# Optimization experiments

Hardware: AMD Instinct MI355X
Metric: run time of the kernel (lower is better)

## Reference

```python
import jax, jax.numpy as jnp
import numpy as np

BS, N, DX, DE, DY, NH = 4, 256, 256, 64, 64, 8
DF = DX // NH


def setup_inputs() -> dict:
    key = jax.random.key(0)
    ks = jax.random.split(key, 24)

    def w(k, i, o):
        return jax.random.normal(k, (i, o), jnp.float32) / jnp.sqrt(jnp.float32(i))

    d = {}
    d["x"] = jax.random.normal(ks[0], (BS, N, DX), jnp.float32)
    d["e"] = jax.random.normal(ks[1], (BS, N, N, DE), jnp.float32)
    d["y"] = jax.random.normal(ks[2], (BS, DY), jnp.float32)
    d["node_mask"] = jnp.ones((BS, N), jnp.float32)
    # projections (use_bias=False in the module)
    d["Wq"] = w(ks[3], DX, DX)
    d["Wk"] = w(ks[4], DX, DX)
    d["Wv"] = w(ks[5], DX, DX)
    d["We_mul"] = w(ks[6], DE, DX)
    d["We_add"] = w(ks[7], DE, DX)
    d["Wye_add"] = w(ks[8], DY, DX)
    d["Wye_mul"] = w(ks[9], DY, DX)
    d["Wyx_add"] = w(ks[10], DY, DX)
    d["Wyx_mul"] = w(ks[11], DY, DX)
    d["Wyy"] = w(ks[12], DY, DY)
    # pooled-feature -> y maps (Xtoy / Etoy use 4*d features: mean,min,max,std)
    d["Wxy"] = w(ks[13], 4 * DX, DY)
    d["bxy"] = jnp.zeros((DY,), jnp.float32)
    d["Wey"] = w(ks[14], 4 * DE, DY)
    d["bey"] = jnp.zeros((DY,), jnp.float32)
    # output heads (bias=True, flax Dense default)
    d["We_out"] = w(ks[15], DX, DE)
    d["be_out"] = jnp.zeros((DE,), jnp.float32)
    d["Wx_out"] = w(ks[16], DX, DX)
    d["bx_out"] = jnp.zeros((DX,), jnp.float32)
    d["Wy_out"] = w(ks[17], DY, DY)
    d["by_out"] = jnp.zeros((DY,), jnp.float32)
    return d


def reference(x, e, y, node_mask, Wq, Wk, Wv, We_mul, We_add, Wye_add, Wye_mul,
              Wyx_add, Wyx_mul, Wyy, Wxy, bxy, Wey, bey, We_out, be_out,
              Wx_out, bx_out, Wy_out, by_out):
    bs, n, dx = x.shape
    nh, df = NH, DF
    x_mask = node_mask[..., None]                       # (bs,n,1)
    e_mask1 = x_mask[:, :, None, :]                     # (bs,n,1,1)
    e_mask2 = x_mask[:, None, :, :]                     # (bs,1,n,1)
    em = e_mask1 * e_mask2                              # (bs,n,n,1)

    q = (x @ Wq) * x_mask
    k = (x @ Wk) * x_mask
    Q = q.reshape(bs, n, 1, nh, df)                     # (bs,n,1,h,df)
    K = k.reshape(bs, 1, n, nh, df)                     # (bs,1,n,h,df)
    Y = Q * K / jnp.sqrt(jnp.float32(df))               # (bs,n,n,h,df) per-channel scores

    e1 = ((e @ We_mul) * em).reshape(bs, n, n, nh, df)
    e2 = ((e @ We_add) * em).reshape(bs, n, n, nh, df)
    Y = Y * (e1 + 1.0) + e2                             # FiLM by edges

    newE = Y.reshape(bs, n, n, dx)
    ye1 = (y @ Wye_add)[:, None, None, :]
    ye2 = (y @ Wye_mul)[:, None, None, :]
    newE = ye1 + (ye2 + 1.0) * newE                     # FiLM by global y
    newE = (newE @ We_out + be_out) * em                # (bs,n,n,de)

    # masked softmax over key axis (axis=2); mask broadcasts over df
    mask5 = e_mask2[..., None] > 0                      # (bs,1,n,1,1)
    attn = jax.nn.softmax(jnp.where(mask5, Y, -1e9), axis=2)

    v = ((x @ Wv) * x_mask).reshape(bs, 1, n, nh, df)
    weighted = (attn * v).sum(axis=2).reshape(bs, n, dx)

    yx1 = (y @ Wyx_add)[:, None, :]
    yx2 = (y @ Wyx_mul)[:, None, :]
    newX = yx1 + (yx2 + 1.0) * weighted
    newX = (newX @ Wx_out + bx_out) * x_mask            # (bs,n,dx)

    def pool(t, axes):
        return jnp.concatenate([t.mean(axis=axes), t.min(axis=axes),
                                t.max(axis=axes), t.std(axis=axes, ddof=1)], axis=-1)

    x_y = pool(x, (1,)) @ Wxy + bxy                     # (bs,dy)
    e_y = pool(e, (1, 2)) @ Wey + bey                   # (bs,dy)
    y_y = y @ Wyy
    newY = (y_y + e_y + x_y) @ Wy_out + by_out          # (bs,dy)
    return newX, newE, newY
```

## Files before the change

kernel.cpp:

```cpp
#include <hip/hip_runtime.h>
#include <hip/hip_bf16.h>

#define BSZ 4
#define NN  256
#define DXX 256
#define DEE 64
#define DYY 64

#define OFF_Q     0
#define OFF_K     262144
#define OFF_V     524288
#define OFF_XW    786432
#define OFF_YE1   1048576
#define OFF_YE2   1049600
#define OFF_YX1   1050624
#define OFF_YX2   1051648
#define OFF_PX    1052672
#define OFF_EPART 1057792

typedef __attribute__((ext_vector_type(8))) short bf16x8;
typedef __attribute__((ext_vector_type(4))) float f32x4;

__device__ __forceinline__ short f2bf(float f) {
    unsigned u = __float_as_uint(f);
    unsigned r = u + 0x7fffu + ((u >> 16) & 1u);
    return (short)(r >> 16);
}

__device__ __forceinline__ unsigned cvt_pk_bf16(float lo, float hi) {
    unsigned r;
    asm("v_cvt_pk_bf16_f32 %0, %1, %2" : "=v"(r) : "v"(lo), "v"(hi));
    return r;
}

__device__ __forceinline__ void pack8_store(const float4& A, const float4& B, short* dst) {
    uint4 v;
    v.x = cvt_pk_bf16(A.x, A.y);
    v.y = cvt_pk_bf16(A.z, A.w);
    v.z = cvt_pk_bf16(B.x, B.y);
    v.w = cvt_pk_bf16(B.z, B.w);
    *(uint4*)dst = v;
}

__global__ __launch_bounds__(256) void prep_kernel(
    const float* __restrict__ x, const float* __restrict__ e, const float* __restrict__ y,
    const float* __restrict__ nm,
    const float* __restrict__ Wq, const float* __restrict__ Wk, const float* __restrict__ Wv,
    const float* __restrict__ Wye_add, const float* __restrict__ Wye_mul,
    const float* __restrict__ Wyx_add, const float* __restrict__ Wyx_mul,
    float* __restrict__ ws) {

    __shared__ float smem[16 * 256];
    const int blk = blockIdx.x;
    const int t = threadIdx.x;

    if (blk < 384) {
        const int which = blk >> 7;
        const int m0 = (blk & 127) * 8;
        const float* W = which == 0 ? Wq : (which == 1 ? Wk : Wv);
        float* out = ws + (size_t)which * 262144;
        float (*xl)[256] = (float(*)[256])smem;
        for (int r = 0; r < 8; ++r) xl[r][t] = x[(m0 + r) * 256 + t];
        __syncthreads();
        float acc[8];
#pragma unroll
        for (int r = 0; r < 8; ++r) acc[r] = 0.f;
        for (int d = 0; d < 256; d += 4) {
            float w0 = W[(d + 0) * 256 + t];
            float w1 = W[(d + 1) * 256 + t];
            float w2 = W[(d + 2) * 256 + t];
            float w3 = W[(d + 3) * 256 + t];
#pragma unroll
            for (int r = 0; r < 8; ++r) {
                float4 ev = *(const float4*)&xl[r][d];
                acc[r] = fmaf(ev.x, w0, fmaf(ev.y, w1, fmaf(ev.z, w2, fmaf(ev.w, w3, acc[r]))));
            }
        }
        if (which == 0) {
#pragma unroll
            for (int r = 0; r < 8; ++r) {
                int m = m0 + r;
                out[m * 256 + t] = acc[r] * nm[m];
            }
        } else {
            const int bb2  = m0 >> 8;
            const int jloc = m0 & 255;
            float tv[8];
#pragma unroll
            for (int r = 0; r < 8; ++r) tv[r] = acc[r] * nm[m0 + r];
            float* outb = out + (size_t)bb2 * 65536 + t * 256 + jloc;
            *(float4*)&outb[0] = make_float4(tv[0], tv[1], tv[2], tv[3]);
            *(float4*)&outb[4] = make_float4(tv[4], tv[5], tv[6], tv[7]);
        }
    } else if (blk < 388) {
        const int b = blk - 384;
        float a1 = 0.f, a2 = 0.f, a3 = 0.f, a4 = 0.f;
        for (int k = 0; k < DYY; ++k) {
            float yv = y[b * DYY + k];
            a1 = fmaf(yv, Wye_add[k * 256 + t], a1);
            a2 = fmaf(yv, Wye_mul[k * 256 + t], a2);
            a3 = fmaf(yv, Wyx_add[k * 256 + t], a3);
            a4 = fmaf(yv, Wyx_mul[k * 256 + t], a4);
        }
        ws[OFF_YE1 + b * 256 + t] = a1;
        ws[OFF_YE2 + b * 256 + t] = a2;
        ws[OFF_YX1 + b * 256 + t] = a3;
        ws[OFF_YX2 + b * 256 + t] = a4;
    } else if (blk < 644) {
        const int idx = blk - 388;
        const int s = idx & 63, bb = idx >> 6;
        const int dq = (t & 15) * 4, g = t >> 4;
        const float* base = e + ((size_t)bb * 65536 + s * 1024) * 64;
        float s0 = 0.f, s1 = 0.f, s2 = 0.f, s3 = 0.f;
        float q0 = 0.f, q1 = 0.f, q2 = 0.f, q3 = 0.f;
        float mn0 = 1e30f, mn1 = 1e30f, mn2 = 1e30f, mn3 = 1e30f;
        float mx0 = -1e30f, mx1 = -1e30f, mx2 = -1e30f, mx3 = -1e30f;
#pragma unroll 4
        for (int rr = 0; rr < 64; ++rr) {
            const int row = g * 64 + rr;
            float4 v = *(const float4*)&base[row * 64 + dq];
            s0 += v.x; s1 += v.y; s2 += v.z; s3 += v.w;
            q0 = fmaf(v.x, v.x, q0); q1 = fmaf(v.y, v.y, q1);
            q2 = fmaf(v.z, v.z, q2); q3 = fmaf(v.w, v.w, q3);
            mn0 = fminf(mn0, v.x); mn1 = fminf(mn1, v.y);
            mn2 = fminf(mn2, v.z); mn3 = fminf(mn3, v.w);
            mx0 = fmaxf(mx0, v.x); mx1 = fmaxf(mx1, v.y);
            mx2 = fmaxf(mx2, v.z); mx3 = fmaxf(mx3, v.w);
        }
        float (*red)[16][64] = (float(*)[16][64])smem;
        red[0][g][dq + 0] = s0;  red[0][g][dq + 1] = s1;  red[0][g][dq + 2] = s2;  red[0][g][dq + 3] = s3;
        red[1][g][dq + 0] = q0;  red[1][g][dq + 1] = q1;  red[1][g][dq + 2] = q2;  red[1][g][dq + 3] = q3;
        red[2][g][dq + 0] = mn0; red[2][g][dq + 1] = mn1; red[2][g][dq + 2] = mn2; red[2][g][dq + 3] = mn3;
        red[3][g][dq + 0] = mx0; red[3][g][dq + 1] = mx1; red[3][g][dq + 2] = mx2; red[3][g][dq + 3] = mx3;
        __syncthreads();
        const int stat = t >> 6, d = t & 63;
        float a;
        if (stat < 2) {
            a = 0.f;
            for (int gg = 0; gg < 16; ++gg) a += red[stat][gg][d];
        } else if (stat == 2) {
            a = 1e30f;
            for (int gg = 0; gg < 16; ++gg) a = fminf(a, red[2][gg][d]);
        } else {
            a = -1e30f;
            for (int gg = 0; gg < 16; ++gg) a = fmaxf(a, red[3][gg][d]);
        }
        ws[OFF_EPART + (size_t)((bb * 64 + s) * 64 + d) * 4 + stat] = a;
    } else {
        const int b = blk - 644;
        float s = 0.f, q = 0.f, mn = 1e30f, mx = -1e30f;
        for (int i = 0; i < 256; ++i) {
            float v = x[(b * 256 + i) * 256 + t];
            s += v; q = fmaf(v, v, q);
            mn = fminf(mn, v); mx = fmaxf(mx, v);
        }
        float mean = s * (1.f / 256.f);
        float var  = (q - s * s * (1.f / 256.f)) * (1.f / 255.f);
        var = fmaxf(var, 0.f);
        ws[OFF_PX + b * 1024 + t]       = mean;
        ws[OFF_PX + b * 1024 + 256 + t] = mn;
        ws[OFF_PX + b * 1024 + 512 + t] = mx;
        ws[OFF_PX + b * 1024 + 768 + t] = sqrtf(var);
    }
}

#define EBP  72
#define YPLP 264

__global__ __launch_bounds__(256, 2) void fusedmfma_kernel(
    const float* __restrict__ e, const float* __restrict__ nmask,
    const float* __restrict__ Wm, const float* __restrict__ Wa,
    const float* __restrict__ We_out, const float* __restrict__ be_out,
    const float* __restrict__ ws, float* __restrict__ outE, float* __restrict__ xw) {

    const int i = blockIdx.x, b = blockIdx.y;
    const int tid  = threadIdx.x;
    const int w    = tid >> 6;
    const int lane = tid & 63;
    const int quad = lane >> 4, l16 = lane & 15;

    __shared__ __align__(16) short ebuf[2][32 * EBP];
    __shared__ __align__(16) short ypl[2][32 * YPLP];
    __shared__ float nml[256];

    nml[tid] = nmask[b * 256 + tid];

    bf16x8 bm[4][2], ba[4][2], bw[8];
    const int cw = w * 64;
#pragma unroll
    for (int ct = 0; ct < 4; ++ct) {
        const int c = cw + ct * 16 + l16;
#pragma unroll
        for (int s = 0; s < 2; ++s) {
            bf16x8 t1, t2;
#pragma unroll
            for (int jj = 0; jj < 8; ++jj) {
                const int d = s * 32 + quad * 8 + jj;
                t1[jj] = f2bf(Wm[d * 256 + c]);
                t2[jj] = f2bf(Wa[d * 256 + c]);
            }
            bm[ct][s] = t1; ba[ct][s] = t2;
        }
    }
    const int cp = w * 16 + l16;
    {
#pragma unroll
        for (int s = 0; s < 8; ++s) {
            bf16x8 t;
#pragma unroll
            for (int jj = 0; jj < 8; ++jj) {
                const int cch = s * 32 + quad * 8 + jj;
                t[jj] = f2bf(We_out[cch * 64 + cp]);
            }
            bw[s] = t;
        }
    }
    const float bo = be_out[cp];

    const float rs = 0.17677669529663687f;
    float qc[4], ye1c[4], ye2c[4];
#pragma unroll
    for (int ct = 0; ct < 4; ++ct) {
        const int c = cw + ct * 16 + l16;
        qc[ct]   = ws[OFF_Q + (size_t)(b * 256 + i) * 256 + c] * rs;
        ye1c[ct] = ws[OFF_YE1 + b * 256 + c];
        ye2c[ct] = ws[OFF_YE2 + b * 256 + c] + 1.f;
    }
    const float* kTb = ws + OFF_K + (size_t)b * 65536;
    const float* vTb = ws + OFF_V + (size_t)b * 65536;

    const float* eb = e + ((size_t)(b * 256 + i)) * 256 * 64;
    const int jr = tid >> 3, c0 = (tid & 7) * 8;
    {
        float4 A = *(const float4*)(eb + jr * 64 + c0);
        float4 B = *(const float4*)(eb + jr * 64 + c0 + 4);
        pack8_store(A, B, &ebuf[0][jr * EBP + c0]);
    }
    __syncthreads();
    const float mi = nml[i];
    const size_t outbase = (size_t)(b * 256 + i) * 256;

    float msm[4], lsm[4], wsm[4];
#pragma unroll
    for (int ct = 0; ct < 4; ++ct) { msm[ct] = -1e30f; lsm[ct] = 0.f; wsm[ct] = 0.f; }

    for (int chunk = 0; chunk < 8; ++chunk) {
        const int cur = chunk & 1, j0 = chunk * 32;

        float4 pfA, pfB;
        if (chunk < 7) {
            const float* nb = eb + (size_t)(j0 + 32 + jr) * 64 + c0;
            pfA = *(const float4*)(nb);
            pfB = *(const float4*)(nb + 4);
        }

        bf16x8 ae[2][2];
#pragma unroll
        for (int jt = 0; jt < 2; ++jt)
#pragma unroll
            for (int s = 0; s < 2; ++s)
                ae[jt][s] = *(const bf16x8*)&ebuf[cur][(jt * 16 + l16) * EBP + s * 32 + quad * 8];

        float emv[8];
#pragma unroll
        for (int jt = 0; jt < 2; ++jt)
#pragma unroll
            for (int r = 0; r < 4; ++r)
                emv[jt * 4 + r] = mi * nml[j0 + jt * 16 + quad * 4 + r];

#pragma unroll
        for (int ct = 0; ct < 4; ++ct) {
            const int c = cw + ct * 16 + l16;

            const float4 K0 = *(const float4*)&kTb[c * 256 + j0 + quad * 4];
            const float4 K1 = *(const float4*)&kTb[c * 256 + j0 + 16 + quad * 4];
            const float4 V0 = *(const float4*)&vTb[c * 256 + j0 + quad * 4];
            const float4 V1 = *(const float4*)&vTb[c * 256 + j0 + 16 + quad * 4];
            const float Ks[8] = {K0.x, K0.y, K0.z, K0.w, K1.x, K1.y, K1.z, K1.w};
            const float Vs[8] = {V0.x, V0.y, V0.z, V0.w, V1.x, V1.y, V1.z, V1.w};

            f32x4 a1_0 = {0.f, 0.f, 0.f, 0.f}, a1_1 = {0.f, 0.f, 0.f, 0.f};
            f32x4 a2_0 = {0.f, 0.f, 0.f, 0.f}, a2_1 = {0.f, 0.f, 0.f, 0.f};
#pragma unroll
            for (int s = 0; s < 2; ++s) {
                a1_0 = __builtin_amdgcn_mfma_f32_16x16x32_bf16(ae[0][s], bm[ct][s], a1_0, 0, 0, 0);
                a1_1 = __builtin_amdgcn_mfma_f32_16x16x32_bf16(ae[1][s], bm[ct][s], a1_1, 0, 0, 0);
                a2_0 = __builtin_amdgcn_mfma_f32_16x16x32_bf16(ae[0][s], ba[ct][s], a2_0, 0, 0, 0);
                a2_1 = __builtin_amdgcn_mfma_f32_16x16x32_bf16(ae[1][s], ba[ct][s], a2_1, 0, 0, 0);
            }

            float Ys[8];
#pragma unroll
            for (int jt = 0; jt < 2; ++jt) {
                float yv[4];
#pragma unroll
                for (int r = 0; r < 4; ++r) {
                    const int u  = jt * 4 + r;
                    const float e1v = (jt == 0) ? a1_0[r] : a1_1[r];
                    const float e2v = (jt == 0) ? a2_0[r] : a2_1[r];
                    const float em = emv[u];
                    const float Yv = fmaf(qc[ct] * Ks[u], fmaf(e1v, em, 1.f), e2v * em);
                    yv[r] = fmaf(ye2c[ct], Yv, ye1c[ct]);
                    Ys[u] = (em > 0.f) ? Yv : -1e9f;
                }
                const int jl0 = jt * 16 + quad * 4;
                unsigned short* yb = (unsigned short*)&ypl[cur][jl0 * YPLP + c];
                const unsigned p01 = cvt_pk_bf16(yv[0], yv[1]);
                const unsigned p23 = cvt_pk_bf16(yv[2], yv[3]);
                yb[0]        = (unsigned short)p01;
                yb[YPLP]     = (unsigned short)(p01 >> 16);
                yb[2 * YPLP] = (unsigned short)p23;
                yb[3 * YPLP] = (unsigned short)(p23 >> 16);
            }
            float cm = Ys[0];
#pragma unroll
            for (int u = 1; u < 8; ++u) cm = fmaxf(cm, Ys[u]);
            const float mnew = fmaxf(msm[ct], cm);
            const float al = __expf(msm[ct] - mnew);
            float sum = 0.f, wsum = 0.f;
#pragma unroll
            for (int u = 0; u < 8; ++u) {
                const float p = __expf(Ys[u] - mnew);
                sum += p; wsum = fmaf(p, Vs[u], wsum);
            }
            lsm[ct] = fmaf(lsm[ct], al, sum);
            wsm[ct] = fmaf(wsm[ct], al, wsum);
            msm[ct] = mnew;
        }

        if (chunk < 7) pack8_store(pfA, pfB, &ebuf[cur ^ 1][jr * EBP + c0]);
        __syncthreads();

        f32x4 acc0 = {0.f, 0.f, 0.f, 0.f}, acc1 = {0.f, 0.f, 0.f, 0.f};
#pragma unroll
        for (int s = 0; s < 8; ++s) {
            bf16x8 a0 = *(const bf16x8*)&ypl[cur][(l16) * YPLP + s * 32 + quad * 8];
            bf16x8 a1 = *(const bf16x8*)&ypl[cur][(16 + l16) * YPLP + s * 32 + quad * 8];
            acc0 = __builtin_amdgcn_mfma_f32_16x16x32_bf16(a0, bw[s], acc0, 0, 0, 0);
            acc1 = __builtin_amdgcn_mfma_f32_16x16x32_bf16(a1, bw[s], acc1, 0, 0, 0);
        }
#pragma unroll
        for (int jt = 0; jt < 2; ++jt)
#pragma unroll
            for (int r = 0; r < 4; ++r) {
                const int jl = jt * 16 + quad * 4 + r;
                const int jg = j0 + jl;
                const float em2 = mi * nml[jg];
                const float av = (jt == 0) ? acc0[r] : acc1[r];
                outE[(outbase + jg) * 64 + cp] = (av + bo) * em2;
            }
    }

#pragma unroll
    for (int ct = 0; ct < 4; ++ct) {
        float m = msm[ct], l = lsm[ct], wv = wsm[ct];
#pragma unroll
        for (int off = 16; off < 64; off <<= 1) {
            const float m2 = __shfl_xor(m, off, 64);
            const float l2 = __shfl_xor(l, off, 64);
            const float w2 = __shfl_xor(wv, off, 64);
            const float mn = fmaxf(m, m2);
            const float s1 = __expf(m - mn), s2 = __expf(m2 - mn);
            l = l * s1 + l2 * s2;
            wv = wv * s1 + w2 * s2;
            m = mn;
        }
        if (quad == 0) {
            const int c = cw + ct * 16 + l16;
            const float weighted = wv / l;
            const float yx1 = ws[OFF_YX1 + b * 256 + c];
            const float yx2 = ws[OFF_YX2 + b * 256 + c] + 1.f;
            xw[(size_t)(b * 256 + i) * 256 + c] = fmaf(yx2, weighted, yx1);
        }
    }
}

__global__ __launch_bounds__(256) void post_kernel(
    const float* __restrict__ xwin, const float* __restrict__ Wx_out,
    const float* __restrict__ bx_out, const float* __restrict__ nm,
    const float* __restrict__ y,
    const float* __restrict__ Wyy, const float* __restrict__ Wxy,
    const float* __restrict__ bxy, const float* __restrict__ Wey,
    const float* __restrict__ bey, const float* __restrict__ Wy_out,
    const float* __restrict__ by_out,
    const float* __restrict__ ws, float* __restrict__ outX, float* __restrict__ outY) {

    __shared__ float smem[16 * 256];
    const int blk = blockIdx.x;
    const int t = threadIdx.x;

    if (blk < 128) {
        const int m0 = blk * 8;
        float (*xl)[256] = (float(*)[256])smem;
        for (int r = 0; r < 8; ++r) xl[r][t] = xwin[(m0 + r) * 256 + t];
        __syncthreads();
        float acc[8];
#pragma unroll
        for (int r = 0; r < 8; ++r) acc[r] = 0.f;
        for (int d = 0; d < 256; d += 4) {
            float w0 = Wx_out[(d + 0) * 256 + t];
            float w1 = Wx_out[(d + 1) * 256 + t];
            float w2 = Wx_out[(d + 2) * 256 + t];
            float w3 = Wx_out[(d + 3) * 256 + t];
#pragma unroll
            for (int r = 0; r < 8; ++r) {
                float4 ev = *(const float4*)&xl[r][d];
                acc[r] = fmaf(ev.x, w0, fmaf(ev.y, w1, fmaf(ev.z, w2, fmaf(ev.w, w3, acc[r]))));
            }
        }
        const float bv = bx_out[t];
#pragma unroll
        for (int r = 0; r < 8; ++r) {
            int m = m0 + r;
            outX[m * 256 + t] = (acc[r] + bv) * nm[m];
        }
    } else {
        const int b = blk - 128;
        const int d = t & 63, g = t >> 6;
        {
            float S = 0.f, Q = 0.f, Mn = 1e30f, Mx = -1e30f;
            for (int ss = g * 16; ss < g * 16 + 16; ++ss) {
                const float* ep = ws + OFF_EPART + ((b * 64 + ss) * 64 + d) * 4;
                float4 p = *(const float4*)ep;
                S += p.x; Q += p.y; Mn = fminf(Mn, p.z); Mx = fmaxf(Mx, p.w);
            }
            float (*red)[4][64] = (float(*)[4][64])smem;
            red[0][g][d] = S; red[1][g][d] = Q; red[2][g][d] = Mn; red[3][g][d] = Mx;
        }
        __syncthreads();
        float* pe = smem + 1024;
        if (g == 0) {
            float (*red)[4][64] = (float(*)[4][64])smem;
            float S = 0.f, Q = 0.f, Mn = 1e30f, Mx = -1e30f;
#pragma unroll
            for (int gg = 0; gg < 4; ++gg) {
                S += red[0][gg][d]; Q += red[1][gg][d];
                Mn = fminf(Mn, red[2][gg][d]); Mx = fmaxf(Mx, red[3][gg][d]);
            }
            const float n = 65536.f;
            float meane = S / n;
            float vare  = (Q - S * S / n) / (n - 1.f);
            vare = fmaxf(vare, 0.f);
            pe[d]       = meane;
            pe[64 + d]  = Mn;
            pe[128 + d] = Mx;
            pe[192 + d] = sqrtf(vare);
        }
        __syncthreads();
        const int o = t & 63, ks = t >> 6;
        float a = 0.f;
        if (ks == 0) {
            a = bxy[o] + bey[o];
            for (int k = 0; k < 64; ++k) a = fmaf(y[b * 64 + k], Wyy[k * 64 + o], a);
        }
        for (int k = ks * 64; k < ks * 64 + 64; ++k) a = fmaf(pe[k], Wey[k * 64 + o], a);
        const float* px = ws + OFF_PX + b * 1024;
        for (int k = ks * 256; k < ks * 256 + 256; ++k) a = fmaf(px[k], Wxy[k * 64 + o], a);
        float* redB = smem + 1280;
        redB[ks * 64 + o] = a;
        __syncthreads();
        float* sy = smem + 1536;
        if (ks == 0) sy[o] = redB[o] + redB[64 + o] + redB[128 + o] + redB[192 + o];
        __syncthreads();
        if (t < 64) {
            float r = by_out[t];
            for (int k = 0; k < 64; ++k) r = fmaf(sy[k], Wy_out[k * 64 + t], r);
            outY[b * 64 + t] = r;
        }
    }
}

extern "C" void kernel_launch(void* const* d_in, const int* in_sizes, int n_in,
                              void* d_out, int out_size, void* d_ws, size_t ws_size,
                              hipStream_t stream) {
    const float* x        = (const float*)d_in[0];
    const float* e        = (const float*)d_in[1];
    const float* y        = (const float*)d_in[2];
    const float* nm       = (const float*)d_in[3];
    const float* Wq       = (const float*)d_in[4];
    const float* Wk       = (const float*)d_in[5];
    const float* Wv       = (const float*)d_in[6];
    const float* We_mul   = (const float*)d_in[7];
    const float* We_add   = (const float*)d_in[8];
    const float* Wye_add  = (const float*)d_in[9];
    const float* Wye_mul  = (const float*)d_in[10];
    const float* Wyx_add  = (const float*)d_in[11];
    const float* Wyx_mul  = (const float*)d_in[12];
    const float* Wyy      = (const float*)d_in[13];
    const float* Wxy      = (const float*)d_in[14];
    const float* bxy      = (const float*)d_in[15];
    const float* Wey      = (const float*)d_in[16];
    const float* bey      = (const float*)d_in[17];
    const float* We_out   = (const float*)d_in[18];
    const float* be_out   = (const float*)d_in[19];
    const float* Wx_out   = (const float*)d_in[20];
    const float* bx_out   = (const float*)d_in[21];
    const float* Wy_out   = (const float*)d_in[22];
    const float* by_out   = (const float*)d_in[23];

    float* ws   = (float*)d_ws;
    float* outX = (float*)d_out;
    float* outE = (float*)d_out + 262144;
    float* outY = (float*)d_out + 262144 + 16777216;

    prep_kernel<<<648, 256, 0, stream>>>(x, e, y, nm, Wq, Wk, Wv,
                                         Wye_add, Wye_mul, Wyx_add, Wyx_mul, ws);
    fusedmfma_kernel<<<dim3(256, 4), 256, 0, stream>>>(e, nm, We_mul, We_add, We_out, be_out,
                                                       ws, outE, ws + OFF_XW);
    post_kernel<<<132, 256, 0, stream>>>(ws + OFF_XW, Wx_out, bx_out, nm, y,
                                         Wyy, Wxy, bxy, Wey, bey, Wy_out, by_out,
                                         ws, outX, outY);
}
```

Measured before the change: 268.2 us.

## Fuse edge pooling statistics into the main MFMA kernel with atomic reduction

Removes the separate pass over the 64MB edge tensor in the prep kernel that computed sum, sum of squares, min and max. These statistics are now accumulated from the e tiles the fused kernel already loads, reduced per block in shared memory, and merged globally with float atomicAdd and order-preserving unsigned atomicMin/Max. The second full read of e goes away. In exchange the fused kernel needs extra registers, which may hurt occupancy, and the atomic float sums make the result order-dependent.

After: 361.8 us. 34.9% more time.

```diff
diff --git a/kernel.cpp b/kernel.cpp
--- a/kernel.cpp
+++ b/kernel.cpp
@@ -42,6 +42,14 @@
     *(uint4*)dst = v;
 }
 
+__device__ __forceinline__ unsigned encf(float f) {
+    unsigned u = __float_as_uint(f);
+    return (u >> 31) ? ~u : (u | 0x80000000u);
+}
+__device__ __forceinline__ float decf(unsigned u) {
+    return __uint_as_float((u >> 31) ? (u & 0x7fffffffu) : ~u);
+}
+
 __global__ __launch_bounds__(256) void prep_kernel(
     const float* __restrict__ x, const float* __restrict__ e, const float* __restrict__ y,
     const float* __restrict__ nm,
@@ -106,48 +114,8 @@
         ws[OFF_YE2 + b * 256 + t] = a2;
         ws[OFF_YX1 + b * 256 + t] = a3;
         ws[OFF_YX2 + b * 256 + t] = a4;
-    } else if (blk < 644) {
-        const int idx = blk - 388;
-        const int s = idx & 63, bb = idx >> 6;
-        const int dq = (t & 15) * 4, g = t >> 4;
-        const float* base = e + ((size_t)bb * 65536 + s * 1024) * 64;
-        float s0 = 0.f, s1 = 0.f, s2 = 0.f, s3 = 0.f;
-        float q0 = 0.f, q1 = 0.f, q2 = 0.f, q3 = 0.f;
-        float mn0 = 1e30f, mn1 = 1e30f, mn2 = 1e30f, mn3 = 1e30f;
-        float mx0 = -1e30f, mx1 = -1e30f, mx2 = -1e30f, mx3 = -1e30f;
-#pragma unroll 4
-        for (int rr = 0; rr < 64; ++rr) {
-            const int row = g * 64 + rr;
-            float4 v = *(const float4*)&base[row * 64 + dq];
-            s0 += v.x; s1 += v.y; s2 += v.z; s3 += v.w;
-            q0 = fmaf(v.x, v.x, q0); q1 = fmaf(v.y, v.y, q1);
-            q2 = fmaf(v.z, v.z, q2); q3 = fmaf(v.w, v.w, q3);
-            mn0 = fminf(mn0, v.x); mn1 = fminf(mn1, v.y);
-            mn2 = fminf(mn2, v.z); mn3 = fminf(mn3, v.w);
-            mx0 = fmaxf(mx0, v.x); mx1 = fmaxf(mx1, v.y);
-            mx2 = fmaxf(mx2, v.z); mx3 = fmaxf(mx3, v.w);
-        }
-        float (*red)[16][64] = (float(*)[16][64])smem;
-        red[0][g][dq + 0] = s0;  red[0][g][dq + 1] = s1;  red[0][g][dq + 2] = s2;  red[0][g][dq + 3] = s3;
-        red[1][g][dq + 0] = q0;  red[1][g][dq + 1] = q1;  red[1][g][dq + 2] = q2;  red[1][g][dq + 3] = q3;
-        red[2][g][dq + 0] = mn0; red[2][g][dq + 1] = mn1; red[2][g][dq + 2] = mn2; red[2][g][dq + 3] = mn3;
-        red[3][g][dq + 0] = mx0; red[3][g][dq + 1] = mx1; red[3][g][dq + 2] = mx2; red[3][g][dq + 3] = mx3;
-        __syncthreads();
-        const int stat = t >> 6, d = t & 63;
-        float a;
-        if (stat < 2) {
-            a = 0.f;
-            for (int gg = 0; gg < 16; ++gg) a += red[stat][gg][d];
-        } else if (stat == 2) {
-            a = 1e30f;
-            for (int gg = 0; gg < 16; ++gg) a = fminf(a, red[2][gg][d]);
-        } else {
-            a = -1e30f;
-            for (int gg = 0; gg < 16; ++gg) a = fmaxf(a, red[3][gg][d]);
-        }
-        ws[OFF_EPART + (size_t)((bb * 64 + s) * 64 + d) * 4 + stat] = a;
-    } else {
-        const int b = blk - 644;
+    } else if (blk < 392) {
+        const int b = blk - 388;
         float s = 0.f, q = 0.f, mn = 1e30f, mx = -1e30f;
         for (int i = 0; i < 256; ++i) {
             float v = x[(b * 256 + i) * 256 + t];
@@ -161,17 +129,29 @@
         ws[OFF_PX + b * 1024 + 256 + t] = mn;
         ws[OFF_PX + b * 1024 + 512 + t] = mx;
         ws[OFF_PX + b * 1024 + 768 + t] = sqrtf(var);
+    } else {
+        float* ep = ws + OFF_EPART;
+        ep[t]       = 0.f;
+        ep[256 + t] = 0.f;
+        ((unsigned*)ep)[512 + t] = 0u;
+        ((unsigned*)ep)[768 + t] = 0xFFFFFFFFu;
     }
 }
 
 #define EBP  72
 #define YPLP 264
+
+#define ESTAT(k, v) { es[k] += (v); eq[k] = fmaf((v), (v), eq[k]); \
+                      emn[k] = fminf(emn[k], (v)); emx[k] = fmaxf(emx[k], (v)); }
+#define ESTAT8(A, B) { ESTAT(0, A.x) ESTAT(1, A.y) ESTAT(2, A.z) ESTAT(3, A.w) \
+                       ESTAT(4, B.x) ESTAT(5, B.y) ESTAT(6, B.z) ESTAT(7, B.w) }
 
 __global__ __launch_bounds__(256, 2) void fusedmfma_kernel(
     const float* __restrict__ e, const float* __restrict__ nmask,
     const float* __restrict__ Wm, const float* __restrict__ Wa,
     const float* __restrict__ We_out, const float* __restrict__ be_out,
-    const float* __restrict__ ws, float* __restrict__ outE, float* __restrict__ xw) {
+    const float* __restrict__ ws, float* __restrict__ outE, float* __restrict__ xw,
+    float* __restrict__ epart) {
 
     const int i = blockIdx.x, b = blockIdx.y;
     const int tid  = threadIdx.x;
@@ -229,11 +209,16 @@
     const float* kTb = ws + OFF_K + (size_t)b * 65536;
     const float* vTb = ws + OFF_V + (size_t)b * 65536;
 
+    float es[8], eq[8], emn[8], emx[8];
+#pragma unroll
+    for (int k = 0; k < 8; ++k) { es[k] = 0.f; eq[k] = 0.f; emn[k] = 1e30f; emx[k] = -1e30f; }
+
     const float* eb = e + ((size_t)(b * 256 + i)) * 256 * 64;
     const int jr = tid >> 3, c0 = (tid & 7) * 8;
     {
         float4 A = *(const float4*)(eb + jr * 64 + c0);
         float4 B = *(const float4*)(eb + jr * 64 + c0 + 4);
+        ESTAT8(A, B)
         pack8_store(A, B, &ebuf[0][jr * EBP + c0]);
     }
     __syncthreads();
@@ -328,7 +313,10 @@
             msm[ct] = mnew;
         }
 
-        if (chunk < 7) pack8_store(pfA, pfB, &ebuf[cur ^ 1][jr * EBP + c0]);
+        if (chunk < 7) {
+            ESTAT8(pfA, pfB)
+            pack8_store(pfA, pfB, &ebuf[cur ^ 1][jr * EBP + c0]);
+        }
         __syncthreads();
 
         f32x4 acc0 = {0.f, 0.f, 0.f, 0.f}, acc1 = {0.f, 0.f, 0.f, 0.f};
@@ -349,6 +337,30 @@
                 const float av = (jt == 0) ? acc0[r] : acc1[r];
                 outE[(outbase + jg) * 64 + cp] = (av + bo) * em2;
             }
+    }
+
+    __syncthreads();
+    {
+        float* sred = (float*)ypl;
+        const int cg = tid & 7;
+        const int jr2 = tid >> 3;
+#pragma unroll
+        for (int k = 0; k < 8; ++k)
+            *(float4*)&sred[jr2 * 260 + (cg * 8 + k) * 4] =
+                make_float4(es[k], eq[k], emn[k], emx[k]);
+        __syncthreads();
+        if (tid < 64) {
+            float4 a = make_float4(0.f, 0.f, 1e30f, -1e30f);
+            for (int j = 0; j < 32; ++j) {
+                float4 v = *(const float4*)&sred[j * 260 + tid * 4];
+                a.x += v.x; a.y += v.y;
+                a.z = fminf(a.z, v.z); a.w = fmaxf(a.w, v.w);
+            }
+            atomicAdd(&epart[b * 64 + tid], a.x);
+            atomicAdd(&epart[256 + b * 64 + tid], a.y);
+            atomicMax((unsigned*)epart + 512 + b * 64 + tid, encf(a.w));
+            atomicMin((unsigned*)epart + 768 + b * 64 + tid, encf(a.z));
+        }
     }
 
 #pragma unroll
@@ -416,35 +428,20 @@
         }
     } else {
         const int b = blk - 128;
-        const int d = t & 63, g = t >> 6;
-        {
-            float S = 0.f, Q = 0.f, Mn = 1e30f, Mx = -1e30f;
-            for (int ss = g * 16; ss < g * 16 + 16; ++ss) {
-                const float* ep = ws + OFF_EPART + ((b * 64 + ss) * 64 + d) * 4;
-                float4 p = *(const float4*)ep;
-                S += p.x; Q += p.y; Mn = fminf(Mn, p.z); Mx = fmaxf(Mx, p.w);
-            }
-            float (*red)[4][64] = (float(*)[4][64])smem;
-            red[0][g][d] = S; red[1][g][d] = Q; red[2][g][d] = Mn; red[3][g][d] = Mx;
-        }
-        __syncthreads();
-        float* pe = smem + 1024;
-        if (g == 0) {
-            float (*red)[4][64] = (float(*)[4][64])smem;
-            float S = 0.f, Q = 0.f, Mn = 1e30f, Mx = -1e30f;
-#pragma unroll
-            for (int gg = 0; gg < 4; ++gg) {
-                S += red[0][gg][d]; Q += red[1][gg][d];
-                Mn = fminf(Mn, red[2][gg][d]); Mx = fmaxf(Mx, red[3][gg][d]);
-            }
+        float* pe = smem;
+        if (t < 64) {
+            const float* ep = ws + OFF_EPART;
+            const float S = ep[b * 64 + t];
+            const float Q = ep[256 + b * 64 + t];
+            const unsigned mxe = ((const unsigned*)ep)[512 + b * 64 + t];
+            const unsigned mne = ((const unsigned*)ep)[768 + b * 64 + t];
             const float n = 65536.f;
             float meane = S / n;
-            float vare  = (Q - S * S / n) / (n - 1.f);
-            vare = fmaxf(vare, 0.f);
-            pe[d]       = meane;
-            pe[64 + d]  = Mn;
-            pe[128 + d] = Mx;
-            pe[192 + d] = sqrtf(vare);
+            float vare  = fmaxf((Q - S * S / n) / (n - 1.f), 0.f);
+            pe[t]       = meane;
+            pe[64 + t]  = decf(mne);
+            pe[128 + t] = decf(mxe);
+            pe[192 + t] = sqrtf(vare);
         }
         __syncthreads();
         const int o = t & 63, ks = t >> 6;
@@ -456,10 +453,10 @@
         for (int k = ks * 64; k < ks * 64 + 64; ++k) a = fmaf(pe[k], Wey[k * 64 + o], a);
         const float* px = ws + OFF_PX + b * 1024;
         for (int k = ks * 256; k < ks * 256 + 256; ++k) a = fmaf(px[k], Wxy[k * 64 + o], a);
-        float* redB = smem + 1280;
+        float* redB = smem + 256;
         redB[ks * 64 + o] = a;
         __syncthreads();
-        float* sy = smem + 1536;
+        float* sy = smem + 512;
         if (ks == 0) sy[o] = redB[o] + redB[64 + o] + redB[128 + o] + redB[192 + o];
         __syncthreads();
         if (t < 64) {
@@ -503,10 +500,11 @@
     float* outE = (float*)d_out + 262144;
     float* outY = (float*)d_out + 262144 + 16777216;
 
-    prep_kernel<<<648, 256, 0, stream>>>(x, e, y, nm, Wq, Wk, Wv,
+    prep_kernel<<<393, 256, 0, stream>>>(x, e, y, nm, Wq, Wk, Wv,
                                          Wye_add, Wye_mul, Wyx_add, Wyx_mul, ws);
     fusedmfma_kernel<<<dim3(256, 4), 256, 0, stream>>>(e, nm, We_mul, We_add, We_out, be_out,
-                                                       ws, outE, ws + OFF_XW);
+                                                       ws, outE, ws + OFF_XW,
+                                                       ws + OFF_EPART);
     post_kernel<<<132, 256, 0, stream>>>(ws + OFF_XW, Wx_out, bx_out, nm, y,
                                          Wyy, Wxy, bxy, Wey, bey, Wy_out, by_out,
                                          ws, outX, outY);
```
